# Kernel tuning notes

Measured on AMD Instinct MI355X. Metric: run time of the kernel, lower is better.

## Reference

```python
import jax, jax.numpy as jnp
import numpy as np

DIM = 1024
NUM_HEADS = 16
HEAD_DIM = DIM // NUM_HEADS


def setup_inputs() -> dict:
    key = jax.random.key(0)
    ks = jax.random.split(key, 5)
    B, T = 2, 2048
    x = jax.random.normal(ks[0], (B, T, DIM), dtype=jnp.float32)
    s = 1.0 / np.sqrt(DIM)
    W_qkv = jax.random.normal(ks[1], (DIM, 3 * DIM), dtype=jnp.float32) * s
    b_qkv = jnp.zeros((3 * DIM,), dtype=jnp.float32)
    W_out = jax.random.normal(ks[2], (DIM, DIM), dtype=jnp.float32) * s
    b_out = jnp.zeros((DIM,), dtype=jnp.float32)
    return {"x": x, "W_qkv": W_qkv, "b_qkv": b_qkv, "W_out": W_out, "b_out": b_out}


def reference(x, W_qkv, b_qkv, W_out, b_out):
    B, T, D = x.shape
    H, Hd = NUM_HEADS, HEAD_DIM
    qkv = x @ W_qkv + b_qkv                       # [B,T,3D]
    qkv = qkv.reshape(B, T, 3, H, Hd)
    q = jnp.transpose(qkv[:, :, 0], (0, 2, 1, 3))  # [B,H,T,Hd]
    k = jnp.transpose(qkv[:, :, 1], (0, 2, 1, 3))
    v = jnp.transpose(qkv[:, :, 2], (0, 2, 1, 3))
    att = jnp.einsum('bhqd,bhkd->bhqk', q, k) / np.sqrt(Hd)  # [B,H,T,T]
    causal = jnp.tril(jnp.ones((T, T), dtype=bool))
    att = jnp.where(causal[None, None], att, -jnp.inf)
    att = jax.nn.softmax(att, axis=-1)
    out = jnp.einsum('bhqk,bhkd->bhqd', att, v)   # [B,H,T,Hd]
    out = jnp.transpose(out, (0, 2, 1, 3)).reshape(B, T, D)
    return out @ W_out + b_out
```

## Files before the change

kernel.cpp:

```cpp
#include <hip/hip_runtime.h>
#include <hip/hip_bf16.h>

typedef unsigned short u16;
typedef __attribute__((ext_vector_type(8))) short short8;
typedef __attribute__((ext_vector_type(4))) float f32x4;
typedef __attribute__((ext_vector_type(4))) unsigned short u16x4;

#define LOG2E 1.44269504088896340736f


__device__ __forceinline__ void gl_lds16(const void* g, void* l) {
  __builtin_amdgcn_global_load_lds(
      (__attribute__((address_space(1))) void*)g,
      (__attribute__((address_space(3))) void*)l, 16, 0, 0);
}

__device__ __forceinline__ float exp2_fast(float x) {
#if __has_builtin(__builtin_amdgcn_exp2f)
  return __builtin_amdgcn_exp2f(x);
#else
  return exp2f(x);
#endif
}

__device__ __forceinline__ u16 f2bf(float f) {
  union { float f; unsigned int i; } v;
  v.f = f;
  unsigned int r = v.i + 0x7fffu + ((v.i >> 16) & 1u);
  return (u16)(r >> 16);
}

__device__ __forceinline__ unsigned int pack_bf2(float lo, float hi) {
  union { __hip_bfloat162 h2; unsigned int u; } c;
  c.h2 = __float22bfloat162_rn(make_float2(lo, hi));
  return c.u;
}


__global__ __launch_bounds__(256) void prep_kernel(
    const float4* __restrict__ x, u16x4* __restrict__ xb,
    const float* __restrict__ Wqkv, u16* __restrict__ WqkvT,
    const float* __restrict__ Wout, u16* __restrict__ WoutT) {
  __shared__ u16 t[64][65];
  int bid = blockIdx.x, tid = threadIdx.x;
  if (bid < 4096) {
    int i = bid * 256 + tid;
    float4 v = x[i];
    u16x4 o;
    o.x = f2bf(v.x); o.y = f2bf(v.y); o.z = f2bf(v.z); o.w = f2bf(v.w);
    xb[i] = o;
    return;
  }
  const float* W;
  u16* WT;
  int K = 1024, N, bxx, byy;
  if (bid < 4864) {
    int tt = bid - 4096;
    W = Wqkv; WT = WqkvT; N = 3072; bxx = tt % 48; byy = tt / 48;
  } else {
    int tt = bid - 4864;
    W = Wout; WT = WoutT; N = 1024; bxx = tt % 16; byy = tt / 16;
  }
  int r0 = byy * 64, c0 = bxx * 64;
  int tx = tid & 63, ty = tid >> 6;
  for (int r = ty; r < 64; r += 4)
    t[r][tx] = f2bf(W[(size_t)(r0 + r) * N + c0 + tx]);
  __syncthreads();
  for (int r = ty; r < 64; r += 4)
    WT[(size_t)(c0 + r) * K + r0 + tx] = t[tx][r];
}


template <bool OUT_F32, int BM, int BN>
__global__ __launch_bounds__(512, 1) void gemm8_kernel(
    const u16* __restrict__ A, const u16* __restrict__ Bt,
    const float* __restrict__ bias, void* __restrict__ Cout,
    int M, int N, int K) {
  constexpr int MI = BM / 32;
  constexpr int NJ = BN / 64;
  constexpr int CH_A = BM / 8;
  constexpr int CH_B = BN / 8;
  constexpr int PER_W = (CH_A + CH_B) / 8;
  __shared__ u16 LDS[2][(BM + BN) * 64];
  int tid = threadIdx.x;
  int w = tid >> 6, lane = tid & 63, l15 = lane & 15, quad = lane >> 4;
  int bid = blockIdx.y * gridDim.x + blockIdx.x;
  int swz = ((bid & 7) << 5) | (bid >> 3);
  int bx = swz % gridDim.x, by = swz / gridDim.x;
  int m0 = by * BM, n0 = bx * BN;
  int wm = (w & 1) * (BM / 2), wn = (w >> 1) * (BN / 4);

  f32x4 acc[MI][NJ];
#pragma unroll
  for (int i = 0; i < MI; ++i)
#pragma unroll
    for (int j = 0; j < NJ; ++j) {
      f32x4 z = {0.f, 0.f, 0.f, 0.f};
      acc[i][j] = z;
    }

  int r8 = lane >> 3;
  int sw = ((lane & 7) ^ r8) * 8;

  const u16* srcp[PER_W];
  int dsto[PER_W];
#pragma unroll
  for (int i = 0; i < PER_W; ++i) {
    int c = w * PER_W + i;
    if (c < CH_A) {
      srcp[i] = A + (size_t)(m0 + c * 8 + r8) * K + sw;
    } else {
      srcp[i] = Bt + (size_t)(n0 + (c - CH_A) * 8 + r8) * K + sw;
    }
    dsto[i] = c * 512;
  }

  int nt = K >> 6;
#pragma unroll
  for (int i = 0; i < PER_W; ++i) gl_lds16(srcp[i], &LDS[0][dsto[i]]);

  for (int t = 0; t < nt; ++t) {
    asm volatile("s_waitcnt vmcnt(0)" ::: "memory");
    __builtin_amdgcn_s_barrier();
    asm volatile("" ::: "memory");
    int cur = t & 1;
    if (t + 1 < nt) {
      int koff = (t + 1) << 6;
#pragma unroll
      for (int i = 0; i < PER_W; ++i)
        gl_lds16(srcp[i] + koff, &LDS[cur ^ 1][dsto[i]]);
    }
    const u16* As = &LDS[cur][0];
    const u16* Bs = &LDS[cur][CH_A * 512];
#pragma unroll
    for (int kh = 0; kh < 2; ++kh) {
      short8 af[MI], bf[NJ];
#pragma unroll
      for (int i = 0; i < MI; ++i) {
        int R = wm + i * 16 + l15;
        af[i] = *(const short8*)(As + R * 64 +
                                 ((kh * 32 + quad * 8) ^ ((R & 7) * 8)));
      }
#pragma unroll
      for (int j = 0; j < NJ; ++j) {
        int R = wn + j * 16 + l15;
        bf[j] = *(const short8*)(Bs + R * 64 +
                                 ((kh * 32 + quad * 8) ^ ((R & 7) * 8)));
      }
#pragma unroll
      for (int i = 0; i < MI; ++i)
#pragma unroll
        for (int j = 0; j < NJ; ++j)
          acc[i][j] = __builtin_amdgcn_mfma_f32_16x16x32_bf16(af[i], bf[j],
                                                              acc[i][j], 0, 0, 0);
    }
  }

  float bv[NJ];
#pragma unroll
  for (int j = 0; j < NJ; ++j) bv[j] = bias[n0 + wn + j * 16 + l15];
#pragma unroll
  for (int i = 0; i < MI; ++i)
#pragma unroll
    for (int j = 0; j < NJ; ++j) {
      int col = n0 + wn + j * 16 + l15;
#pragma unroll
      for (int r = 0; r < 4; ++r) {
        int row = m0 + wm + i * 16 + quad * 4 + r;
        float val = acc[i][j][r] + bv[j];
        if (OUT_F32)
          ((float*)Cout)[(size_t)row * N + col] = val;
        else
          ((u16*)Cout)[(size_t)row * N + col] = f2bf(val);
      }
    }
}


__global__ __launch_bounds__(512, 2) void flash_kernel(
    const u16* __restrict__ qkv, u16* __restrict__ att) {
  __shared__ unsigned int SH[28672];

  int tid = threadIdx.x;
  int w = tid >> 6, half = w >> 2, wq = w & 3;
  int lane = tid & 63, l15 = lane & 15, quad = lane >> 4;
  int bx = blockIdx.x;
  int p = bx >> 5, bh = bx & 31, b = bh >> 4, h = bh & 15;
  const int qs[2] = {15 - p, p};
  const int kmax0 = 2 * qs[0] + 1, kmax1 = 2 * p + 1;
  const int jmax = 16 - p;

  const u16* base = qkv + (size_t)b * 2048 * 3072 + h * 64;
  const u16* kb = base + 1024;
  const u16* vb = base + 2048;

  int ht = tid & 255;
  const int krow = ht >> 3, h7 = ht & 7;
  const int swk = (h7 ^ (krow & 7)) * 8;

  short8 qf[2][2][2];
#pragma unroll
  for (int t = 0; t < 2; ++t) {
    const u16* qtb = base + (size_t)(qs[t] * 128 + wq * 32 + l15) * 3072;
    qf[t][0][0] = *(const short8*)(qtb + quad * 8);
    qf[t][0][1] = *(const short8*)(qtb + 32 + quad * 8);
    qf[t][1][0] = *(const short8*)(qtb + 16 * 3072 + quad * 8);
    qf[t][1][1] = *(const short8*)(qtb + 16 * 3072 + 32 + quad * 8);
  }

  {
    unsigned int* Ks0 = SH + half * 2048;
    gl_lds16(kb + (size_t)(half * 64 + krow) * 3072 + swk,
             (char*)Ks0 + wq * 1024);
    gl_lds16(kb + (size_t)(half * 64 + 32 + krow) * 3072 + swk,
             (char*)Ks0 + 4096 + wq * 1024);
  }
  uint4 vr0 = *(const uint4*)(vb + (size_t)(half * 64 + 2 * krow) * 3072 + h7 * 8);
  uint4 vr1 = *(const uint4*)(vb + (size_t)(half * 64 + 2 * krow + 1) * 3072 + h7 * 8);

  f32x4 o[2][2][4];
#pragma unroll
  for (int t = 0; t < 2; ++t)
#pragma unroll
    for (int qsub = 0; qsub < 2; ++qsub)
#pragma unroll
      for (int jd = 0; jd < 4; ++jd) {
        f32x4 z = {0.f, 0.f, 0.f, 0.f};
        o[t][qsub][jd] = z;
      }
  float lsum[2][2] = {0.f, 0.f, 0.f, 0.f};

  const int psw = (l15 & 7) << 2;
  const float kscale = 0.125f * LOG2E;
  unsigned int* Pw = SH + 20480 + w * 1024;

  int b3 = 0;
  for (int j = 0; j < jmax; ++j) {
    int kt = 2 * j + half;
    unsigned int* KsH = SH + b3 * 4096 + half * 2048;
    unsigned int* VtH = SH + 12288 + (j & 1) * 4096 + half * 2048;

    {
      const u16* av = (const u16*)&vr0;
      const u16* bvp = (const u16*)&vr1;
#pragma unroll
      for (int jj = 0; jj < 8; ++jj) {
        int d = h7 * 8 + jj;
        VtH[32 * d + (krow ^ ((jj ^ h7) << 2))] =
            (unsigned int)av[jj] | ((unsigned int)bvp[jj] << 16);
      }
    }

    int nb3 = b3 + 1;
    if (nb3 == 3) nb3 = 0;
    if (j + 1 < jmax) {
      int kn = (kt + 2) * 64;
      unsigned int* Ksn = SH + nb3 * 4096 + half * 2048;
      gl_lds16(kb + (size_t)(kn + krow) * 3072 + swk, (char*)Ksn + wq * 1024);
      gl_lds16(kb + (size_t)(kn + 32 + krow) * 3072 + swk,
               (char*)Ksn + 4096 + wq * 1024);
      vr0 = *(const uint4*)(vb + (size_t)(kn + 2 * krow) * 3072 + h7 * 8);
      vr1 = *(const uint4*)(vb + (size_t)(kn + 2 * krow + 1) * 3072 + h7 * 8);
    }
    b3 = nb3;

    asm volatile("s_waitcnt lgkmcnt(0)" ::: "memory");
    __builtin_amdgcn_s_barrier();
    asm volatile("" ::: "memory");

#pragma unroll
    for (int t = 0; t < 2; ++t) {
      int km = t ? kmax1 : kmax0;
      if (kt > km) continue;
      bool last = (kt == km);
      if (last && wq < 2) continue;
      bool domask = last || ((kt == km - 1) && wq < 2);
      int qloc = ((last ? (wq - 2) : wq) << 5) + l15;

      f32x4 s0[4], s1[4];
#pragma unroll
      for (int jn = 0; jn < 4; ++jn) {
        f32x4 z = {0.f, 0.f, 0.f, 0.f};
        s0[jn] = z;
        s1[jn] = z;
      }
      __builtin_amdgcn_s_setprio(1);
#pragma unroll
      for (int ss = 0; ss < 2; ++ss) {
        short8 a0 = qf[t][0][ss];
        short8 a1 = qf[t][1][ss];
#pragma unroll
        for (int jn = 0; jn < 4; ++jn) {
          int row = jn * 16 + l15;
          short8 bk = *(const short8*)&KsH[32 * row + ((16 * ss + 4 * quad) ^
                                                       ((row & 7) << 2))];
          s0[jn] = __builtin_amdgcn_mfma_f32_16x16x32_bf16(bk, a0, s0[jn], 0, 0, 0);
          s1[jn] = __builtin_amdgcn_mfma_f32_16x16x32_bf16(bk, a1, s1[jn], 0, 0, 0);
        }
      }
      __builtin_amdgcn_s_setprio(0);

#pragma unroll
      for (int qsub = 0; qsub < 2; ++qsub) {
        int qq = qloc + qsub * 16;
        float pvv[4][4];
        if (domask) {
#pragma unroll
          for (int jn = 0; jn < 4; ++jn) {
            f32x4 sv = qsub ? s1[jn] : s0[jn];
#pragma unroll
            for (int r = 0; r < 4; ++r) {
              float e = exp2_fast(fmaf(sv[r], kscale, -16.0f));
              if (jn * 16 + quad * 4 + r > qq) e = 0.f;
              pvv[jn][r] = e;
            }
          }
        } else {
#pragma unroll
          for (int jn = 0; jn < 4; ++jn) {
            f32x4 sv = qsub ? s1[jn] : s0[jn];
#pragma unroll
            for (int r = 0; r < 4; ++r)
              pvv[jn][r] = exp2_fast(fmaf(sv[r], kscale, -16.0f));
          }
        }
        float t0 = (pvv[0][0] + pvv[0][1]) + (pvv[0][2] + pvv[0][3]);
        float t1 = (pvv[1][0] + pvv[1][1]) + (pvv[1][2] + pvv[1][3]);
        float t2 = (pvv[2][0] + pvv[2][1]) + (pvv[2][2] + pvv[2][3]);
        float t3 = (pvv[3][0] + pvv[3][1]) + (pvv[3][2] + pvv[3][3]);
        lsum[t][qsub] += (t0 + t1) + (t2 + t3);
#pragma unroll
        for (int jn = 0; jn < 4; ++jn) {
          uint2 dd = make_uint2(pack_bf2(pvv[jn][0], pvv[jn][1]),
                                pack_bf2(pvv[jn][2], pvv[jn][3]));
          *(uint2*)&Pw[qsub * 512 + 32 * l15 +
                       (((jn << 3) + (quad << 1)) ^ psw)] = dd;
        }
      }

      __builtin_amdgcn_s_setprio(1);
#pragma unroll
      for (int ss = 0; ss < 2; ++ss) {
        short8 pf0 = *(const short8*)&Pw[32 * l15 +
                                         (((ss << 4) + (quad << 2)) ^ psw)];
        short8 pf1 = *(const short8*)&Pw[512 + 32 * l15 +
                                         (((ss << 4) + (quad << 2)) ^ psw)];
#pragma unroll
        for (int jd = 0; jd < 4; ++jd) {
          int vrow = jd * 16 + l15;
          int f = (vrow & 7) ^ ((vrow >> 3) & 7);
          short8 bvv = *(const short8*)&VtH[32 * vrow +
                                            (((ss << 4) + (quad << 2)) ^ (f << 2))];
          o[t][0][jd] =
              __builtin_amdgcn_mfma_f32_16x16x32_bf16(bvv, pf0, o[t][0][jd], 0, 0, 0);
          o[t][1][jd] =
              __builtin_amdgcn_mfma_f32_16x16x32_bf16(bvv, pf1, o[t][1][jd], 0, 0, 0);
        }
      }
      __builtin_amdgcn_s_setprio(0);
    }
  }

  float lf[2][2];
#pragma unroll
  for (int t = 0; t < 2; ++t)
#pragma unroll
    for (int qsub = 0; qsub < 2; ++qsub) {
      float v = lsum[t][qsub];
      v += __shfl_xor(v, 16, 64);
      v += __shfl_xor(v, 32, 64);
      lf[t][qsub] = v;
    }

  float* OM = (float*)SH;
  float* LM = (float*)(SH + 8704);
  __syncthreads();
#pragma unroll
  for (int t = 0; t < 2; ++t) {
    if (half == 0) {
#pragma unroll
      for (int qsub = 0; qsub < 2; ++qsub) {
        int q = wq * 32 + qsub * 16 + l15;
#pragma unroll
        for (int jd = 0; jd < 4; ++jd)
          *(float4*)&OM[q * 68 + jd * 16 + quad * 4] = *(float4*)&o[t][qsub][jd];
        if (quad == 0) LM[q] = lf[t][qsub];
      }
    }
    __syncthreads();
    if (half == 1) {
#pragma unroll
      for (int qsub = 0; qsub < 2; ++qsub) {
        int q = wq * 32 + qsub * 16 + l15;
        float lr = lf[t][qsub] + LM[q];
        float inv = 1.f / lr;
        size_t row = (size_t)b * 2048 + qs[t] * 128 + q;
        u16* orow = att + row * 1024 + h * 64 + quad * 4;
#pragma unroll
        for (int jd = 0; jd < 4; ++jd) {
          float4 pa = *(float4*)&OM[q * 68 + jd * 16 + quad * 4];
          uint2 dd = make_uint2(pack_bf2((o[t][qsub][jd][0] + pa.x) * inv,
                                         (o[t][qsub][jd][1] + pa.y) * inv),
                                pack_bf2((o[t][qsub][jd][2] + pa.z) * inv,
                                         (o[t][qsub][jd][3] + pa.w) * inv));
          *(uint2*)(orow + jd * 16) = dd;
        }
      }
    }
    __syncthreads();
  }
}


extern "C" void kernel_launch(void* const* d_in, const int* in_sizes, int n_in,
                              void* d_out, int out_size, void* d_ws,
                              size_t ws_size, hipStream_t stream) {
  const float* x = (const float*)d_in[0];
  const float* Wqkv = (const float*)d_in[1];
  const float* bqkv = (const float*)d_in[2];
  const float* Wout = (const float*)d_in[3];
  const float* bout = (const float*)d_in[4];
  float* out = (float*)d_out;

  char* ws = (char*)d_ws;
  u16* WqkvT = (u16*)(ws);
  u16* WoutT = (u16*)(ws + 6291456);
  u16* qkv = (u16*)(ws + 8388608);
  u16* attn = (u16*)(ws + 33554432);
  u16* xb = (u16*)(ws + 41943040);

  prep_kernel<<<5120, 256, 0, stream>>>((const float4*)x, (u16x4*)xb, Wqkv,
                                        WqkvT, Wout, WoutT);
  gemm8_kernel<false, 256, 192><<<dim3(16, 16), 512, 0, stream>>>(
      xb, WqkvT, bqkv, (void*)qkv, 4096, 3072, 1024);
  flash_kernel<<<256, 512, 0, stream>>>(qkv, attn);
  gemm8_kernel<true, 128, 128><<<dim3(8, 32), 512, 0, stream>>>(
      attn, WoutT, bout, (void*)out, 4096, 1024, 1024);
}
```

Before: 163.4 us.

## Write V transposed from QKV GEMM epilogue and DMA it directly into flash LDS

The QKV GEMM epilogue now writes the V columns in a per-head transposed [B,H,Hd,T] layout, using a small LDS shuffle so each lane stores 8-byte contiguous runs. The flash kernel then loads V^T tiles with async global-to-LDS loads, the same way it loads K. This removes the register round trip and scattered LDS transpose of V inside the attention loop, and lets a double-buffered K/V scheme replace the triple-buffered one with less LDS. The cost is extra epilogue work and an extra workspace buffer. The loop also now waits on vmcnt at the top of each iteration, which may expose load latency.

```diff
diff --git a/kernel.cpp b/kernel.cpp
--- a/kernel.cpp
+++ b/kernel.cpp
@@ -71,11 +71,11 @@
 }
 
 
-template <bool OUT_F32, int BM, int BN>
+template <bool OUT_F32, int BM, int BN, bool VSPLIT>
 __global__ __launch_bounds__(512, 1) void gemm8_kernel(
     const u16* __restrict__ A, const u16* __restrict__ Bt,
     const float* __restrict__ bias, void* __restrict__ Cout,
-    int M, int N, int K) {
+    u16* __restrict__ Vt, int M, int N, int K) {
   constexpr int MI = BM / 32;
   constexpr int NJ = BN / 64;
   constexpr int CH_A = BM / 8;
@@ -163,23 +163,38 @@
   for (int i = 0; i < MI; ++i)
 #pragma unroll
     for (int j = 0; j < NJ; ++j) {
-      int col = n0 + wn + j * 16 + l15;
-#pragma unroll
-      for (int r = 0; r < 4; ++r) {
-        int row = m0 + wm + i * 16 + quad * 4 + r;
-        float val = acc[i][j][r] + bv[j];
-        if (OUT_F32)
-          ((float*)Cout)[(size_t)row * N + col] = val;
-        else
-          ((u16*)Cout)[(size_t)row * N + col] = f2bf(val);
+      if (VSPLIT && n0 + wn + j * 16 >= 2048) {
+        uint2* scr = (uint2*)&LDS[0][w * 256];
+        uint2 pk;
+        pk.x = pack_bf2(acc[i][j][0] + bv[j], acc[i][j][1] + bv[j]);
+        pk.y = pack_bf2(acc[i][j][2] + bv[j], acc[i][j][3] + bv[j]);
+        scr[l15 * 4 + quad] = pk;
+        uint2 vv = scr[(lane >> 2) * 4 + (lane & 3)];
+        int hd = n0 + wn + j * 16 + (lane >> 2) - 2048;
+        int mr = m0 + wm + i * 16;
+        int bb = mr >> 11;
+        int t0 = (mr & 2047) + (lane & 3) * 4;
+        *(uint2*)(Vt + ((size_t)(bb * 1024 + hd) << 11) + t0) = vv;
+      } else {
+        int col = n0 + wn + j * 16 + l15;
+#pragma unroll
+        for (int r = 0; r < 4; ++r) {
+          int row = m0 + wm + i * 16 + quad * 4 + r;
+          float val = acc[i][j][r] + bv[j];
+          if (OUT_F32)
+            ((float*)Cout)[(size_t)row * N + col] = val;
+          else
+            ((u16*)Cout)[(size_t)row * N + col] = f2bf(val);
+        }
       }
     }
 }
 
 
 __global__ __launch_bounds__(512, 2) void flash_kernel(
-    const u16* __restrict__ qkv, u16* __restrict__ att) {
-  __shared__ unsigned int SH[28672];
+    const u16* __restrict__ qkv, const u16* __restrict__ vT,
+    u16* __restrict__ att) {
+  __shared__ unsigned int SH[24576];
 
   int tid = threadIdx.x;
   int w = tid >> 6, half = w >> 2, wq = w & 3;
@@ -192,11 +207,14 @@
 
   const u16* base = qkv + (size_t)b * 2048 * 3072 + h * 64;
   const u16* kb = base + 1024;
-  const u16* vb = base + 2048;
+  const u16* vbT = vT + (size_t)(b * 16 + h) * 131072;
 
   int ht = tid & 255;
   const int krow = ht >> 3, h7 = ht & 7;
   const int swk = (h7 ^ (krow & 7)) * 8;
+  const int fk = (krow & 7) ^ ((krow >> 3) & 7);
+  const u16* v0 = vbT + (size_t)krow * 2048 + ((h7 ^ fk) << 3);
+  const u16* v1 = vbT + (size_t)(32 + krow) * 2048 + (((h7 ^ fk) ^ 4) << 3);
 
   short8 qf[2][2][2];
 #pragma unroll
@@ -210,13 +228,14 @@
 
   {
     unsigned int* Ks0 = SH + half * 2048;
+    unsigned int* Vt0 = SH + 8192 + half * 2048;
     gl_lds16(kb + (size_t)(half * 64 + krow) * 3072 + swk,
              (char*)Ks0 + wq * 1024);
     gl_lds16(kb + (size_t)(half * 64 + 32 + krow) * 3072 + swk,
              (char*)Ks0 + 4096 + wq * 1024);
-  }
-  uint4 vr0 = *(const uint4*)(vb + (size_t)(half * 64 + 2 * krow) * 3072 + h7 * 8);
-  uint4 vr1 = *(const uint4*)(vb + (size_t)(half * 64 + 2 * krow + 1) * 3072 + h7 * 8);
+    gl_lds16(v0 + half * 64, (char*)Vt0 + wq * 1024);
+    gl_lds16(v1 + half * 64, (char*)Vt0 + 4096 + wq * 1024);
+  }
 
   f32x4 o[2][2][4];
 #pragma unroll
@@ -232,41 +251,27 @@
 
   const int psw = (l15 & 7) << 2;
   const float kscale = 0.125f * LOG2E;
-  unsigned int* Pw = SH + 20480 + w * 1024;
-
-  int b3 = 0;
+  unsigned int* Pw = SH + 16384 + w * 1024;
+
   for (int j = 0; j < jmax; ++j) {
     int kt = 2 * j + half;
-    unsigned int* KsH = SH + b3 * 4096 + half * 2048;
-    unsigned int* VtH = SH + 12288 + (j & 1) * 4096 + half * 2048;
-
-    {
-      const u16* av = (const u16*)&vr0;
-      const u16* bvp = (const u16*)&vr1;
-#pragma unroll
-      for (int jj = 0; jj < 8; ++jj) {
-        int d = h7 * 8 + jj;
-        VtH[32 * d + (krow ^ ((jj ^ h7) << 2))] =
-            (unsigned int)av[jj] | ((unsigned int)bvp[jj] << 16);
-      }
-    }
-
-    int nb3 = b3 + 1;
-    if (nb3 == 3) nb3 = 0;
+    unsigned int* KsH = SH + (j & 1) * 4096 + half * 2048;
+    unsigned int* VtH = SH + 8192 + (j & 1) * 4096 + half * 2048;
+
+    asm volatile("s_waitcnt vmcnt(0)" ::: "memory");
+    __builtin_amdgcn_s_barrier();
+    asm volatile("" ::: "memory");
+
     if (j + 1 < jmax) {
       int kn = (kt + 2) * 64;
-      unsigned int* Ksn = SH + nb3 * 4096 + half * 2048;
+      unsigned int* Ksn = SH + ((j + 1) & 1) * 4096 + half * 2048;
+      unsigned int* Vtn = SH + 8192 + ((j + 1) & 1) * 4096 + half * 2048;
       gl_lds16(kb + (size_t)(kn + krow) * 3072 + swk, (char*)Ksn + wq * 1024);
       gl_lds16(kb + (size_t)(kn + 32 + krow) * 3072 + swk,
                (char*)Ksn + 4096 + wq * 1024);
-      vr0 = *(const uint4*)(vb + (size_t)(kn + 2 * krow) * 3072 + h7 * 8);
-      vr1 = *(const uint4*)(vb + (size_t)(kn + 2 * krow + 1) * 3072 + h7 * 8);
-    }
-    b3 = nb3;
-
-    asm volatile("s_waitcnt lgkmcnt(0)" ::: "memory");
-    __builtin_amdgcn_s_barrier();
-    asm volatile("" ::: "memory");
+      gl_lds16(v0 + kn, (char*)Vtn + wq * 1024);
+      gl_lds16(v1 + kn, (char*)Vtn + 4096 + wq * 1024);
+    }
 
 #pragma unroll
     for (int t = 0; t < 2; ++t) {
@@ -428,12 +433,13 @@
   u16* qkv = (u16*)(ws + 8388608);
   u16* attn = (u16*)(ws + 33554432);
   u16* xb = (u16*)(ws + 41943040);
+  u16* vt = (u16*)(ws + 50331648);
 
   prep_kernel<<<5120, 256, 0, stream>>>((const float4*)x, (u16x4*)xb, Wqkv,
                                         WqkvT, Wout, WoutT);
-  gemm8_kernel<false, 256, 192><<<dim3(16, 16), 512, 0, stream>>>(
-      xb, WqkvT, bqkv, (void*)qkv, 4096, 3072, 1024);
-  flash_kernel<<<256, 512, 0, stream>>>(qkv, attn);
-  gemm8_kernel<true, 128, 128><<<dim3(8, 32), 512, 0, stream>>>(
-      attn, WoutT, bout, (void*)out, 4096, 1024, 1024);
-}
+  gemm8_kernel<false, 256, 192, true><<<dim3(16, 16), 512, 0, stream>>>(
+      xb, WqkvT, bqkv, (void*)qkv, vt, 4096, 3072, 1024);
+  flash_kernel<<<256, 512, 0, stream>>>(qkv, vt, attn);
+  gemm8_kernel<true, 128, 128, false><<<dim3(8, 32), 512, 0, stream>>>(
+      attn, WoutT, bout, (void*)out, nullptr, 4096, 1024, 1024);
+}
```

New measurement: 164.5 us. No clear change (+0.7%).
